# Kernel tuning notes

Measured on AMD Instinct MI355X. Metric: run time of the kernel, lower is better.

The kernel has to match this reference:

```python
import jax, jax.numpy as jnp
import numpy as np

D_MODEL, D_KEY, N_HEADS = 256, 32, 8
B, T1, T2 = 4, 2048, 2048


def setup_inputs() -> dict:
    key = jax.random.key(0)
    ks = jax.random.split(key, 12)
    s = 1.0 / np.sqrt(D_MODEL)
    inp = {
        "key_input": jax.random.normal(ks[0], (B, T1, D_MODEL), jnp.float32),
        "query_input": jax.random.normal(ks[1], (B, T2, D_MODEL), jnp.float32),
        "value_input": jax.random.normal(ks[2], (B, T1, D_MODEL), jnp.float32),
        "attention_mask": jnp.ones((B, T1, T2), dtype=jnp.bool_),  # unused by the module, kept for API fidelity
        "WK_w": jax.random.uniform(ks[3], (D_KEY * N_HEADS, D_MODEL), jnp.float32, -s, s),
        "WK_b": jax.random.uniform(ks[4], (D_KEY * N_HEADS,), jnp.float32, -s, s),
        "WQ_w": jax.random.uniform(ks[5], (D_KEY * N_HEADS, D_MODEL), jnp.float32, -s, s),
        "WQ_b": jax.random.uniform(ks[6], (D_KEY * N_HEADS,), jnp.float32, -s, s),
        "WV_w": jax.random.uniform(ks[7], (D_MODEL * N_HEADS, D_MODEL), jnp.float32, -s, s),
        "WV_b": jax.random.uniform(ks[8], (D_MODEL * N_HEADS,), jnp.float32, -s, s),
        "WO_w": jax.random.uniform(ks[9], (D_MODEL, D_MODEL * N_HEADS), jnp.float32, -1.0 / np.sqrt(D_MODEL * N_HEADS), 1.0 / np.sqrt(D_MODEL * N_HEADS)),
        "WO_b": jax.random.uniform(ks[10], (D_MODEL,), jnp.float32, -1.0 / np.sqrt(D_MODEL * N_HEADS), 1.0 / np.sqrt(D_MODEL * N_HEADS)),
    }
    return inp


def reference(key_input, query_input, value_input, attention_mask,
              WK_w, WK_b, WQ_w, WQ_b, WV_w, WV_b, WO_w, WO_b):
    b, t1, dm = key_input.shape
    t2 = query_input.shape[1]
    h, dk = N_HEADS, D_KEY
    # projections
    k = key_input @ WK_w.T + WK_b      # [b, t1, h*dk]
    q = query_input @ WQ_w.T + WQ_b    # [b, t2, h*dk]
    v = value_input @ WV_w.T + WV_b    # [b, t1, h*dm] (per-head value dim == d_model)
    # head split: channel index c = head*dk + feat (head outer), matching torch reshapes
    k = k.reshape(b, t1, h, dk)
    q = q.reshape(b, t2, h, dk)
    v = v.reshape(b, t1, h, dm)
    # scores: NO 1/sqrt(dk) scaling and NO masking (faithful to source; mask arg unused)
    scores = jnp.einsum('bshk,bqhk->bhsq', k, q)      # [b, h, t1, t2]
    attn = jax.nn.softmax(scores, axis=2)             # softmax over KEY axis (torch dim=1 of [t1,t2])
    emb = jnp.einsum('bshd,bhsq->bqdh', v, attn)      # [b, t2, dm, h]
    emb = emb.reshape(b, t2, dm * h)                  # flatten (d_model outer, head inner)
    return emb @ WO_w.T + WO_b                        # [b, t2, d_model]
```

## Files before the change

### kernel.cpp

```cpp
#include <hip/hip_runtime.h>

typedef __attribute__((ext_vector_type(8))) short short8;
typedef __attribute__((ext_vector_type(4))) short short4v;
typedef __attribute__((ext_vector_type(4))) float float4v;
typedef __attribute__((ext_vector_type(4))) unsigned uint4v;
typedef __attribute__((ext_vector_type(2))) unsigned uint2v;
typedef __attribute__((ext_vector_type(4))) _Float16 half4;

constexpr int T  = 2048;
constexpr int DM = 256;
constexpr int DK = 32;

__device__ inline short f2bf(float f) {
  unsigned u = __builtin_bit_cast(unsigned, f);
  u += 0x7fff + ((u >> 16) & 1);
  return (short)(u >> 16);
}

__device__ inline unsigned pk2(float a, float b) {
#if __has_builtin(__builtin_amdgcn_cvt_pk_bf16_f32)
  auto r = __builtin_amdgcn_cvt_pk_bf16_f32(a, b);
  return __builtin_bit_cast(unsigned, r);
#else
  unsigned ua = __builtin_bit_cast(unsigned, a);
  ua = (ua + 0x7fff + ((ua >> 16) & 1)) >> 16;
  unsigned ub = __builtin_bit_cast(unsigned, b);
  ub = (ub + 0x7fff + ((ub >> 16) & 1)) >> 16;
  return ua | (ub << 16);
#endif
}

__device__ inline float fexp2(float x) {
#if __has_builtin(__builtin_amdgcn_exp2f)
  return __builtin_amdgcn_exp2f(x);
#else
  return exp2f(x);
#endif
}

__device__ inline short8 load8_bf(const float* __restrict__ p) {
  float4v a = *(const float4v*)p;
  float4v b = *(const float4v*)(p + 4);
  uint4v u;
  u[0] = pk2(a[0], a[1]); u[1] = pk2(a[2], a[3]);
  u[2] = pk2(b[0], b[1]); u[3] = pk2(b[2], b[3]);
  return __builtin_bit_cast(short8, u);
}


__device__ inline void proj_body(const float* __restrict__ A,
                                 const float* __restrict__ Bw,
                                 const float* __restrict__ bias,
                                 short* __restrict__ C, float oscale,
                                 int bx, int by,
                                 short (&As)[128][40], short (&Bs)[128][40]) {
  const int tid  = threadIdx.x;
  const int wave = tid >> 6, lane = tid & 63;
  const int l15  = lane & 15, quad = lane >> 4;
  const int wm   = (wave & 1) * 64, wn = (wave >> 1) * 32;
  const long Abase = (long)bx * 128;
  const long Bbase = (long)by * 64;

  float4v acc[4][2];
  for (int i = 0; i < 4; i++)
    for (int j = 0; j < 2; j++)
      for (int r = 0; r < 4; r++) acc[i][j][r] = 0.f;

  const int srow = tid >> 2;
  const int sc8  = (tid & 3) * 8;

  for (int k0 = 0; k0 < 256; k0 += 32) {
    __syncthreads();
    for (int i = 0; i < 2; i++) {
      int row = srow + i * 64;
      *(short8*)&As[row][sc8] = load8_bf(A + (Abase + row) * 256 + k0 + sc8);
    }
    *(short8*)&Bs[srow][sc8] = load8_bf(Bw + (Bbase + srow) * 256 + k0 + sc8);
    __syncthreads();
    short8 af[4], bfr[2];
    for (int ms = 0; ms < 4; ms++) af[ms]  = *(const short8*)&As[wm + ms*16 + l15][quad*8];
    for (int ns = 0; ns < 2; ns++) bfr[ns] = *(const short8*)&Bs[wn + ns*16 + l15][quad*8];
    for (int ms = 0; ms < 4; ms++)
      for (int ns = 0; ns < 2; ns++)
        acc[ms][ns] = __builtin_amdgcn_mfma_f32_16x16x32_bf16(af[ms], bfr[ns], acc[ms][ns], 0, 0, 0);
  }

  for (int ms = 0; ms < 4; ms++) {
    int rowl = wm + ms*16 + quad*4;
    for (int ns = 0; ns < 2; ns++) {
      int col = (int)Bbase + wn + ns*16 + l15;
      float bv = bias[col];
      for (int r = 0; r < 4; r++) {
        long row = Abase + rowl + r;
        C[row * 256 + col] = f2bf((acc[ms][ns][r] + bv) * oscale);
      }
    }
  }
}

__device__ inline void wf_body(const float* __restrict__ WO_w,
                               const float* __restrict__ WV_w,
                               short* __restrict__ Wf,
                               int h, int bx, int by,
                               short (&As)[128][40], short (&Bs)[128][40]) {
  const int tid  = threadIdx.x;
  const int wave = tid >> 6, lane = tid & 63;
  const int l15  = lane & 15, quad = lane >> 4;
  const int wm   = (wave & 1) * 64, wn = (wave >> 1) * 32;
  const int srow = tid >> 2, sc8 = (tid & 3) * 8;

  float4v acc[4][2];
  for (int i = 0; i < 4; i++)
    for (int j = 0; j < 2; j++)
      for (int r = 0; r < 4; r++) acc[i][j][r] = 0.f;

  for (int d0 = 0; d0 < 256; d0 += 32) {
    __syncthreads();
    for (int i = 0; i < 2; i++) {
      int row = srow + i * 64;
      for (int j = 0; j < 8; j++)
        As[row][sc8 + j] = f2bf(WO_w[(bx*128 + row) * 2048 + (d0 + sc8 + j) * 8 + h]);
    }
    for (int j = 0; j < 8; j++)
      Bs[srow][sc8 + j] = f2bf(WV_w[((h*256) + d0 + sc8 + j) * 256 + by*64 + srow]);
    __syncthreads();
    short8 af[4], bfr[2];
    for (int ms = 0; ms < 4; ms++) af[ms]  = *(const short8*)&As[wm + ms*16 + l15][quad*8];
    for (int ns = 0; ns < 2; ns++) bfr[ns] = *(const short8*)&Bs[wn + ns*16 + l15][quad*8];
    for (int ms = 0; ms < 4; ms++)
      for (int ns = 0; ns < 2; ns++)
        acc[ms][ns] = __builtin_amdgcn_mfma_f32_16x16x32_bf16(af[ms], bfr[ns], acc[ms][ns], 0, 0, 0);
  }
  for (int ms = 0; ms < 4; ms++) {
    int m = bx*128 + wm + ms*16 + quad*4;
    for (int ns = 0; ns < 2; ns++) {
      int col = by*64 + wn + ns*16 + l15;
      for (int r = 0; r < 4; r++)
        Wf[((long)h*256 + m + r) * 256 + col] = f2bf(acc[ms][ns][r]);
    }
  }
}

__device__ inline void ut_body(const short* __restrict__ Wf,
                               const float* __restrict__ Bw,
                               const float* __restrict__ cbias,
                               short* __restrict__ Ut,
                               int bx, int by,
                               short (&As)[128][40], short (&Bs)[128][40]) {
  const int tid  = threadIdx.x;
  const int wave = tid >> 6, lane = tid & 63;
  const int l15  = lane & 15, quad = lane >> 4;
  const int wm   = (wave & 1) * 64, wn = (wave >> 1) * 64;
  const long Abase = (long)bx * 128;
  const long Bbase = (long)by * 128;

  float4v acc[4][4];
  for (int i = 0; i < 4; i++)
    for (int j = 0; j < 4; j++)
      for (int r = 0; r < 4; r++) acc[i][j][r] = 0.f;

  const int srow = tid >> 2;
  const int sc8  = (tid & 3) * 8;

  for (int k0 = 0; k0 < 256; k0 += 32) {
    __syncthreads();
    for (int i = 0; i < 2; i++) {
      int row = srow + i * 64;
      *(short8*)&As[row][sc8] = *(const short8*)(Wf + (Abase + row) * 256 + k0 + sc8);
      *(short8*)&Bs[row][sc8] = load8_bf(Bw + (Bbase + row) * 256 + k0 + sc8);
    }
    __syncthreads();
    short8 af[4], bfr[4];
    for (int ms = 0; ms < 4; ms++) af[ms]  = *(const short8*)&As[wm + ms*16 + l15][quad*8];
    for (int ns = 0; ns < 4; ns++) bfr[ns] = *(const short8*)&Bs[wn + ns*16 + l15][quad*8];
    for (int ms = 0; ms < 4; ms++)
      for (int ns = 0; ns < 4; ns++)
        acc[ms][ns] = __builtin_amdgcn_mfma_f32_16x16x32_bf16(af[ms], bfr[ns], acc[ms][ns], 0, 0, 0);
  }

  for (int ms = 0; ms < 4; ms++) {
    int rowl = wm + ms*16 + quad*4;
    for (int ns = 0; ns < 4; ns++) {
      int col = (int)Bbase + wn + ns*16 + l15;
      int bidx = col >> 11, scol = col & 2047;
      for (int r = 0; r < 4; r++) {
        long m = Abase + rowl + r;
        Ut[((long)bidx * 2048 + m) * 2048 + scol] = f2bf(acc[ms][ns][r] + cbias[m]);
      }
    }
  }
}

__global__ __launch_bounds__(256)
void prep1(const float* __restrict__ WV_w, const float* __restrict__ WV_b,
           const float* __restrict__ WO_w,
           short* __restrict__ Wf, float* __restrict__ cbias) {
  __shared__ __align__(16) short As[128][40];
  __shared__ __align__(16) short Bs[128][40];
  __shared__ float cb_s[16][17];
  const int gb  = blockIdx.x;
  const int tid = threadIdx.x;

  if (gb < 64) {
    wf_body(WO_w, WV_w, Wf, gb >> 3, (gb >> 2) & 1, gb & 3, As, Bs);
  } else {
    const int idx = gb - 64;
    const int h = idx >> 4, ng = idx & 15;
    const int ni = tid & 15, di = tid >> 4;
    const int n = ng * 16 + ni;
    float acc = 0.f;
    for (int j = 0; j < 16; j++) {
      int d = di * 16 + j;
      acc += WV_b[h*256 + d] * WO_w[n * 2048 + d*8 + h];
    }
    cb_s[ni][di] = acc;
    __syncthreads();
    if (tid < 16) {
      float s = 0.f;
      for (int d2 = 0; d2 < 16; d2++) s += cb_s[tid][d2];
      cbias[h*256 + ng*16 + tid] = s;
    }
  }
}

__global__ __launch_bounds__(256)
void front(const float* __restrict__ key_x, const float* __restrict__ query_x,
           const float* __restrict__ value_x,
           const float* __restrict__ WK_w, const float* __restrict__ WK_b,
           const float* __restrict__ WQ_w, const float* __restrict__ WQ_b,
           const short* __restrict__ Wf, const float* __restrict__ cbias,
           short* __restrict__ Kp, short* __restrict__ Qp,
           short* __restrict__ Ut) {
  __shared__ __align__(16) short As[128][40];
  __shared__ __align__(16) short Bs[128][40];
  const int gb = blockIdx.x;

  if (gb < 1024) {
    ut_body(Wf, value_x, cbias, Ut, gb & 15, gb >> 4, As, Bs);
  } else if (gb < 1280) {
    const int g = gb - 1024;
    proj_body(key_x, WK_w, WK_b, Kp, 1.0f, g & 63, g >> 6, As, Bs);
  } else {
    const int g = gb - 1280;
    proj_body(query_x, WQ_w, WQ_b, Qp, 1.44269504f, g & 63, g >> 6, As, Bs);
  }
}

__global__ __launch_bounds__(256, 2)
void attn_kernel(const short* __restrict__ Kp, const short* __restrict__ Qp,
                 const short* __restrict__ Ut, _Float16* __restrict__ partial) {
  __shared__ __align__(16) short Pt[2][128][136];
  __shared__ __align__(16) float psum[128][4];

  const int tid  = threadIdx.x;
  const int wave = tid >> 6, lane = tid & 63;
  const int l15  = lane & 15, quad = lane >> 4;

  const int L  = blockIdx.x;
  const int h  = L & 7;
  const int b  = (L >> 3) & 3;
  const int q0 = (L >> 5) * 128;

  const short* Kbh = Kp + (long)b * T * DM + h * DK;
  const short* Qbh = Qp + (long)b * T * DM + h * DK;
  const short* Ubh = Ut + ((long)b * 2048 + h * 256) * 2048;

  float4v acc[4][8];
  for (int i = 0; i < 4; i++)
    for (int j = 0; j < 8; j++)
      for (int r = 0; r < 4; r++) acc[i][j][r] = 0.f;

  float ps[8];
  for (int i = 0; i < 8; i++) ps[i] = 0.f;

  short8 qf[8];
  for (int qs = 0; qs < 8; qs++)
    qf[qs] = *(const short8*)(Qbh + (long)(q0 + qs*16 + l15) * DM + quad*8);

  auto computeSt = [&](int s0, int buf) {
    for (int ss = 0; ss < 2; ss++) {
      short8 kf = *(const short8*)(Kbh + (long)(s0 + wave*32 + ss*16 + l15) * DM + quad*8);
      for (int qs = 0; qs < 8; qs++) {
        float4v z = {0.f, 0.f, 0.f, 0.f};
        float4v st = __builtin_amdgcn_mfma_f32_16x16x32_bf16(kf, qf[qs], z, 0, 0, 0);
        float p0 = fexp2(st[0]), p1 = fexp2(st[1]);
        float p2 = fexp2(st[2]), p3 = fexp2(st[3]);
        ps[qs] += (p0 + p1) + (p2 + p3);
        uint2v pb; pb[0] = pk2(p0, p1); pb[1] = pk2(p2, p3);
        *(uint2v*)&Pt[buf][qs*16 + l15][wave*32 + ss*16 + quad*4] = pb;
      }
    }
  };

  computeSt(0, 0);

  for (int it = 0; it < T / 128; it++) {
    const int buf = it & 1;
    const int s0  = it * 128;
    __syncthreads();
    if (it < T / 128 - 1) computeSt(s0 + 128, buf ^ 1);
    for (int ks = 0; ks < 4; ks++) {
      short8 pf[8];
      for (int ns = 0; ns < 8; ns++)
        pf[ns] = *(const short8*)&Pt[buf][ns*16 + l15][ks*32 + quad*8];
      for (int ms = 0; ms < 4; ms++) {
        short8 vf = *(const short8*)(Ubh + (long)(wave*64 + ms*16 + l15) * 2048
                                     + s0 + ks*32 + quad*8);
        for (int ns = 0; ns < 8; ns++)
          acc[ms][ns] = __builtin_amdgcn_mfma_f32_16x16x32_bf16(vf, pf[ns], acc[ms][ns], 0, 0, 0);
      }
    }
  }

  for (int qs = 0; qs < 8; qs++) {
    ps[qs] += __shfl_xor(ps[qs], 16, 64);
    ps[qs] += __shfl_xor(ps[qs], 32, 64);
  }
  if (lane < 16)
    for (int qs = 0; qs < 8; qs++) psum[qs*16 + lane][wave] = ps[qs];
  __syncthreads();

  for (int ns = 0; ns < 8; ns++) {
    float4v sv = *(const float4v*)&psum[ns*16 + l15][0];
    float rl = 1.0f / (sv[0] + sv[1] + sv[2] + sv[3]);
    long pbase = ((long)h * 8192 + b * T + q0 + ns*16 + l15) * 256;
    for (int ms = 0; ms < 4; ms++) {
      int ncol = wave*64 + ms*16 + quad*4;
      half4 hv;
      for (int r = 0; r < 4; r++) hv[r] = (_Float16)(acc[ms][ns][r] * rl);
      *(half4*)(partial + pbase + ncol) = hv;
    }
  }
}

__global__ void reduce_out(const _Float16* __restrict__ partial,
                           const float* __restrict__ WO_b,
                           float* __restrict__ out) {
  const long HP = 8192L * 256;
  long i4 = ((long)blockIdx.x * 256 + threadIdx.x) * 4;
  float4v o = *(const float4v*)(WO_b + (i4 & 255));
  for (int h = 0; h < 8; h++) {
    half4 hv = *(const half4*)(partial + h * HP + i4);
    for (int r = 0; r < 4; r++) o[r] += (float)hv[r];
  }
  *(float4v*)(out + i4) = o;
}

extern "C" void kernel_launch(void* const* d_in, const int* in_sizes, int n_in,
                              void* d_out, int out_size, void* d_ws, size_t ws_size,
                              hipStream_t stream) {
  const float* key_x   = (const float*)d_in[0];
  const float* query_x = (const float*)d_in[1];
  const float* value_x = (const float*)d_in[2];
  const float* WK_w = (const float*)d_in[4];
  const float* WK_b = (const float*)d_in[5];
  const float* WQ_w = (const float*)d_in[6];
  const float* WQ_b = (const float*)d_in[7];
  const float* WV_w = (const float*)d_in[8];
  const float* WV_b = (const float*)d_in[9];
  const float* WO_w = (const float*)d_in[10];
  const float* WO_b = (const float*)d_in[11];

  char* ws = (char*)d_ws;
  short*     Kp    = (short*)(ws);
  short*     Qp    = (short*)(ws + (4u  << 20));
  short*     Ut    = (short*)(ws + (8u  << 20));
  short*     Wf    = (short*)(ws + (40u << 20));
  float*     cbias = (float*)(ws + (41u << 20));
  _Float16*  part  = (_Float16*)(ws + (42u << 20));
  float*     outp  = (float*)d_out;

  prep1<<<192, 256, 0, stream>>>(WV_w, WV_b, WO_w, Wf, cbias);
  front<<<1536, 256, 0, stream>>>(key_x, query_x, value_x,
                                  WK_w, WK_b, WQ_w, WQ_b,
                                  Wf, cbias, Kp, Qp, Ut);
  attn_kernel<<<512, 256, 0, stream>>>(Kp, Qp, Ut, part);
  reduce_out<<<2048, 256, 0, stream>>>(part, WO_b, outp);
}
```

Before: 304.1 us.

## Fuse all stages into one persistent kernel with software grid barriers

Replaces the four launches (weight prep, projections, attention, output reduction) with a single 512-block kernel that runs each stage in turn and separates them with atomic-counter grid barriers. The shared-memory buffers of the stages are overlaid in a union. The aim is to remove launch gaps and kernel-boundary drains and to overlap the weight prep with the K/Q projections. In exchange, all 512 blocks must be co-resident for the spin barrier not to deadlock, the barrier spins add latency, and the Ut stage now runs at lower parallelism because each block loops over two tiles instead of 1024 blocks running at once.

```diff
diff --git a/kernel.cpp b/kernel.cpp
--- a/kernel.cpp
+++ b/kernel.cpp
@@ -45,6 +45,25 @@
   u[0] = pk2(a[0], a[1]); u[1] = pk2(a[2], a[3]);
   u[2] = pk2(b[0], b[1]); u[3] = pk2(b[2], b[3]);
   return __builtin_bit_cast(short8, u);
+}
+
+__device__ inline void grid_barrier(unsigned* cnt, unsigned* flag) {
+  __syncthreads();
+  if (threadIdx.x == 0) {
+    __threadfence();
+    unsigned a = atomicAdd(cnt, 1u);
+    if (a == 511u) {
+      atomicExch(flag, 1u);
+    } else {
+      while (atomicAdd(flag, 0u) == 0u) {
+#if __has_builtin(__builtin_amdgcn_s_sleep)
+        __builtin_amdgcn_s_sleep(8);
+#endif
+      }
+    }
+    __threadfence();
+  }
+  __syncthreads();
 }
 
 
@@ -191,72 +210,15 @@
   }
 }
 
-__global__ __launch_bounds__(256)
-void prep1(const float* __restrict__ WV_w, const float* __restrict__ WV_b,
-           const float* __restrict__ WO_w,
-           short* __restrict__ Wf, float* __restrict__ cbias) {
-  __shared__ __align__(16) short As[128][40];
-  __shared__ __align__(16) short Bs[128][40];
-  __shared__ float cb_s[16][17];
-  const int gb  = blockIdx.x;
-  const int tid = threadIdx.x;
-
-  if (gb < 64) {
-    wf_body(WO_w, WV_w, Wf, gb >> 3, (gb >> 2) & 1, gb & 3, As, Bs);
-  } else {
-    const int idx = gb - 64;
-    const int h = idx >> 4, ng = idx & 15;
-    const int ni = tid & 15, di = tid >> 4;
-    const int n = ng * 16 + ni;
-    float acc = 0.f;
-    for (int j = 0; j < 16; j++) {
-      int d = di * 16 + j;
-      acc += WV_b[h*256 + d] * WO_w[n * 2048 + d*8 + h];
-    }
-    cb_s[ni][di] = acc;
-    __syncthreads();
-    if (tid < 16) {
-      float s = 0.f;
-      for (int d2 = 0; d2 < 16; d2++) s += cb_s[tid][d2];
-      cbias[h*256 + ng*16 + tid] = s;
-    }
-  }
-}
-
-__global__ __launch_bounds__(256)
-void front(const float* __restrict__ key_x, const float* __restrict__ query_x,
-           const float* __restrict__ value_x,
-           const float* __restrict__ WK_w, const float* __restrict__ WK_b,
-           const float* __restrict__ WQ_w, const float* __restrict__ WQ_b,
-           const short* __restrict__ Wf, const float* __restrict__ cbias,
-           short* __restrict__ Kp, short* __restrict__ Qp,
-           short* __restrict__ Ut) {
-  __shared__ __align__(16) short As[128][40];
-  __shared__ __align__(16) short Bs[128][40];
-  const int gb = blockIdx.x;
-
-  if (gb < 1024) {
-    ut_body(Wf, value_x, cbias, Ut, gb & 15, gb >> 4, As, Bs);
-  } else if (gb < 1280) {
-    const int g = gb - 1024;
-    proj_body(key_x, WK_w, WK_b, Kp, 1.0f, g & 63, g >> 6, As, Bs);
-  } else {
-    const int g = gb - 1280;
-    proj_body(query_x, WQ_w, WQ_b, Qp, 1.44269504f, g & 63, g >> 6, As, Bs);
-  }
-}
-
-__global__ __launch_bounds__(256, 2)
-void attn_kernel(const short* __restrict__ Kp, const short* __restrict__ Qp,
-                 const short* __restrict__ Ut, _Float16* __restrict__ partial) {
-  __shared__ __align__(16) short Pt[2][128][136];
-  __shared__ __align__(16) float psum[128][4];
-
+__device__ inline void attn_body(const short* __restrict__ Kp,
+                                 const short* __restrict__ Qp,
+                                 const short* __restrict__ Ut,
+                                 _Float16* __restrict__ partial, int L,
+                                 short (&Pt)[2][128][136], float (&psum)[128][4]) {
   const int tid  = threadIdx.x;
   const int wave = tid >> 6, lane = tid & 63;
   const int l15  = lane & 15, quad = lane >> 4;
 
-  const int L  = blockIdx.x;
   const int h  = L & 7;
   const int b  = (L >> 3) & 3;
   const int q0 = (L >> 5) * 128;
@@ -333,17 +295,72 @@
   }
 }
 
-__global__ void reduce_out(const _Float16* __restrict__ partial,
-                           const float* __restrict__ WO_b,
-                           float* __restrict__ out) {
+__global__ __launch_bounds__(256, 2)
+void mega(const float* __restrict__ key_x, const float* __restrict__ query_x,
+          const float* __restrict__ value_x,
+          const float* __restrict__ WK_w, const float* __restrict__ WK_b,
+          const float* __restrict__ WQ_w, const float* __restrict__ WQ_b,
+          const float* __restrict__ WV_w, const float* __restrict__ WV_b,
+          const float* __restrict__ WO_w, const float* __restrict__ WO_b,
+          short* __restrict__ Kp, short* __restrict__ Qp,
+          short* __restrict__ Ut, short* __restrict__ Wf,
+          float* __restrict__ cbias, _Float16* __restrict__ part,
+          float* __restrict__ outp, unsigned* __restrict__ bar) {
+  union SMem {
+    struct { short As[128][40]; short Bs[128][40]; } g;
+    struct { short Pt[2][128][136]; float psum[128][4]; } a;
+    float cb[16][17];
+  };
+  __shared__ __align__(16) SMem sm;
+
+  const int gb  = blockIdx.x;
+  const int tid = threadIdx.x;
+
+  if (gb < 256)
+    proj_body(key_x, WK_w, WK_b, Kp, 1.0f, gb & 63, gb >> 6, sm.g.As, sm.g.Bs);
+  else
+    proj_body(query_x, WQ_w, WQ_b, Qp, 1.44269504f,
+              (gb - 256) & 63, (gb - 256) >> 6, sm.g.As, sm.g.Bs);
+  __syncthreads();
+  if (gb < 64) {
+    wf_body(WO_w, WV_w, Wf, gb >> 3, (gb >> 2) & 1, gb & 3, sm.g.As, sm.g.Bs);
+  } else if (gb < 192) {
+    const int idx = gb - 64;
+    const int h = idx >> 4, ng = idx & 15;
+    const int ni = tid & 15, di = tid >> 4;
+    const int n = ng * 16 + ni;
+    float acc = 0.f;
+    for (int j = 0; j < 16; j++) {
+      int d = di * 16 + j;
+      acc += WV_b[h*256 + d] * WO_w[n * 2048 + d*8 + h];
+    }
+    sm.cb[ni][di] = acc;
+    __syncthreads();
+    if (tid < 16) {
+      float s = 0.f;
+      for (int d2 = 0; d2 < 16; d2++) s += sm.cb[tid][d2];
+      cbias[h*256 + ng*16 + tid] = s;
+    }
+  }
+  grid_barrier(bar + 0, bar + 1);
+
+  for (int jj = gb; jj < 1024; jj += 512)
+    ut_body(Wf, value_x, cbias, Ut, jj & 15, jj >> 4, sm.g.As, sm.g.Bs);
+  grid_barrier(bar + 2, bar + 3);
+
+  attn_body(Kp, Qp, Ut, part, gb, sm.a.Pt, sm.a.psum);
+  grid_barrier(bar + 4, bar + 5);
+
   const long HP = 8192L * 256;
-  long i4 = ((long)blockIdx.x * 256 + threadIdx.x) * 4;
-  float4v o = *(const float4v*)(WO_b + (i4 & 255));
-  for (int h = 0; h < 8; h++) {
-    half4 hv = *(const half4*)(partial + h * HP + i4);
-    for (int r = 0; r < 4; r++) o[r] += (float)hv[r];
-  }
-  *(float4v*)(out + i4) = o;
+  for (int it = 0; it < 4; it++) {
+    long i4 = ((long)gb * 1024 + it * 256 + tid) * 4;
+    float4v o = *(const float4v*)(WO_b + (i4 & 255));
+    for (int h = 0; h < 8; h++) {
+      half4 hv = *(const half4*)(part + h * HP + i4);
+      for (int r = 0; r < 4; r++) o[r] += (float)hv[r];
+    }
+    *(float4v*)(outp + i4) = o;
+  }
 }
 
 extern "C" void kernel_launch(void* const* d_in, const int* in_sizes, int n_in,
@@ -367,13 +384,13 @@
   short*     Ut    = (short*)(ws + (8u  << 20));
   short*     Wf    = (short*)(ws + (40u << 20));
   float*     cbias = (float*)(ws + (41u << 20));
+  unsigned*  bar   = (unsigned*)(ws + (41u << 20) + (64u << 10));
   _Float16*  part  = (_Float16*)(ws + (42u << 20));
   float*     outp  = (float*)d_out;
 
-  prep1<<<192, 256, 0, stream>>>(WV_w, WV_b, WO_w, Wf, cbias);
-  front<<<1536, 256, 0, stream>>>(key_x, query_x, value_x,
-                                  WK_w, WK_b, WQ_w, WQ_b,
-                                  Wf, cbias, Kp, Qp, Ut);
-  attn_kernel<<<512, 256, 0, stream>>>(Kp, Qp, Ut, part);
-  reduce_out<<<2048, 256, 0, stream>>>(part, WO_b, outp);
-}
+  hipMemsetAsync(bar, 0, 64, stream);
+  mega<<<512, 256, 0, stream>>>(key_x, query_x, value_x,
+                                WK_w, WK_b, WQ_w, WQ_b, WV_w, WV_b,
+                                WO_w, WO_b, Kp, Qp, Ut, Wf, cbias,
+                                part, outp, bar);
+}
```

Result: slower. 482.8 us (+58.8%).
